# Kernel optimization log

Hardware: AMD Instinct MI355X
Metric: run time of the kernel (lower is better)

The kernel has to match this reference:

```python
import jax, jax.numpy as jnp
import numpy as np

D = H = W = 64
N = D * H * W
BS = 2
C = 32          # enc_dim
IN_DIM = 4
OUT_DIM = 4
P = 5           # pos_enc_dim
COND = 32
M = 8           # modes per axis
NL = 4          # n_layers
NODE_IN = IN_DIM + 3 + 2 * P * 3   # 37
ENC_T = 1 + 2 * P                  # 11
ENC_C = ENC_T * COND               # 352
DT = 0.05


def fourier_embedding(pos, n_freq):
    # F(x) = [cos(2^i*pi*x_l), sin(2^i*pi*x_l)] per coordinate l, then concat x
    freq = (2.0 ** jnp.arange(n_freq, dtype=jnp.float32)) * jnp.pi  # (P,)
    ang = pos[..., None] * freq                                     # (..., L, P)
    emb = jnp.concatenate([jnp.cos(ang), jnp.sin(ang)], axis=-1)    # (..., L, 2P)
    emb = emb.reshape(*pos.shape[:-1], -1)                          # (..., L*2P)
    return jnp.concatenate([emb, pos], axis=-1)


def setup_inputs() -> dict:
    key = jax.random.key(0)
    ks = jax.random.split(key, 24)
    scale = 1.0 / C ** 2
    inp = {
        "state_in": jax.random.normal(ks[0], (BS, N, IN_DIM), jnp.float32),
        "node_pos": jax.random.uniform(ks[1], (BS, N, 3), jnp.float32),
        "edges": jax.random.randint(ks[2], (BS, 16, 2), 0, N),
        "time_i": jax.random.uniform(ks[3], (BS, 1), jnp.float32),
        "conditions": jax.random.uniform(ks[4], (BS, COND), jnp.float32),
        "t_embed_w": jax.random.normal(ks[5], (C, ENC_T), jnp.float32) * 0.05,
        "t_embed_b": jax.random.normal(ks[6], (C,), jnp.float32) * 0.05,
        "c_embed_w": jax.random.normal(ks[7], (C, ENC_C), jnp.float32) * 0.05,
        "c_embed_b": jax.random.normal(ks[8], (C,), jnp.float32) * 0.05,
        "lift_w": jax.random.normal(ks[9], (C, NODE_IN), jnp.float32) * 0.05,
        "lift_b": jax.random.normal(ks[10], (C,), jnp.float32) * 0.05,
        "spec_wr": jax.random.uniform(ks[11], (NL, C, C, M, M, M), jnp.float32) * scale,
        "spec_wi": jax.random.uniform(ks[12], (NL, C, C, M, M, M), jnp.float32) * scale,
        "byp_w": jax.random.normal(ks[13], (NL, C, C), jnp.float32) * 0.05,
        "byp_b": jax.random.normal(ks[14], (NL, C), jnp.float32) * 0.05,
        "proj1_w": jax.random.normal(ks[15], (C, C), jnp.float32) * 0.05,
        "proj1_b": jax.random.normal(ks[16], (C,), jnp.float32) * 0.05,
        "proj2_w": jax.random.normal(ks[17], (OUT_DIM, C), jnp.float32) * 0.05,
        "proj2_b": jax.random.normal(ks[18], (OUT_DIM,), jnp.float32) * 0.05,
    }
    return inp


def _conv1x1(x, w, b):
    # x: (b, c, d, h, w), w: (o, c), b: (o,)
    return jnp.einsum('bcdhw,oc->bodhw', x, w) + b[None, :, None, None, None]


def _fno_forward(state_in, node_pos, time_i, conditions,
                 t_embed_w, t_embed_b, c_embed_w, c_embed_b, lift_w, lift_b,
                 spec_wr, spec_wi, byp_w, byp_b, proj1_w, proj1_b, proj2_w, proj2_b):
    pos_enc = fourier_embedding(node_pos, P)      # (bs, N, 33)
    c_enc = fourier_embedding(conditions, P)      # (bs, 352)
    t_enc = fourier_embedding(time_i, P)          # (bs, 11)

    node_feat = jnp.concatenate([state_in, pos_enc], axis=-1)  # (bs, N, 37)
    t_emb = (t_enc @ t_embed_w.T + t_embed_b)[:, :, None, None, None]
    c_emb = (c_enc @ c_embed_w.T + c_embed_b)[:, :, None, None, None]

    # (bs, N, 37) -> (bs, 37, D, H, W)
    x = node_feat.transpose(0, 2, 1).reshape(BS, NODE_IN, D, H, W)
    x = _conv1x1(x, lift_w, lift_b)
    x = x + t_emb + c_emb

    for l in range(NL):
        w = jax.lax.complex(spec_wr[l], spec_wi[l])              # (C, C, M, M, M)
        x_ft = jnp.fft.rfftn(x, axes=(-3, -2, -1))               # (bs, C, D, H, W//2+1)
        blk = jnp.einsum('bixyz,ioxyz->boxyz', x_ft[..., :M, :M, :M], w)
        out_ft = jnp.zeros_like(x_ft).at[..., :M, :M, :M].set(blk)
        sp = jnp.fft.irfftn(out_ft, s=(D, H, W), axes=(-3, -2, -1))
        bp = _conv1x1(x, byp_w[l], byp_b[l])
        x = jax.nn.gelu(sp + bp, approximate=False)

    x = jax.nn.gelu(_conv1x1(x, proj1_w, proj1_b), approximate=False)
    x = _conv1x1(x, proj2_w, proj2_b)                            # (bs, 4, D, H, W)
    v_pred = x.reshape(BS, OUT_DIM, N).transpose(0, 2, 1)        # (bs, N, 4)
    return state_in + DT * v_pred


def reference(state_in, node_pos, edges, time_i, conditions,
              t_embed_w, t_embed_b, c_embed_w, c_embed_b, lift_w, lift_b,
              spec_wr, spec_wi, byp_w, byp_b, proj1_w, proj1_b, proj2_w, proj2_b):
    # edges are unused in the FNO forward (kept for API compatibility)
    return _fno_forward(state_in, node_pos, time_i, conditions,
                        t_embed_w, t_embed_b, c_embed_w, c_embed_b, lift_w, lift_b,
                        spec_wr, spec_wi, byp_w, byp_b, proj1_w, proj1_b, proj2_w, proj2_b)
```

## Files before the change

### kernel.cpp

```cpp
#include <hip/hip_runtime.h>
#include <math.h>

#define PI_F 3.14159265358979323846f

typedef __bf16 bf16x8 __attribute__((ext_vector_type(8)));
typedef float floatx4 __attribute__((ext_vector_type(4)));
union U8 { unsigned short u[8]; uint4 q; bf16x8 v; };

__device__ __forceinline__ float gelu_sig(float v) {
    float e = __builtin_amdgcn_exp2f(-2.4554670f * v);
    return v * __builtin_amdgcn_rcpf(1.0f + e);
}
__device__ __forceinline__ int rfl(int x) { return __builtin_amdgcn_readfirstlane(x); }

__device__ __forceinline__ unsigned short f2bf(float f) {
    unsigned int u = __float_as_uint(f);
    u += 0x7fffu + ((u >> 16) & 1u);
    return (unsigned short)(u >> 16);
}
__device__ __forceinline__ float bf2f(unsigned short h) {
    return __uint_as_float(((unsigned int)h) << 16);
}
__device__ __forceinline__ unsigned int pack2(float a, float b) {
    return (unsigned int)f2bf(a) | ((unsigned int)f2bf(b) << 16);
}

__global__ void k_wt(const float* __restrict__ time_i, const float* __restrict__ conditions,
                     const float* __restrict__ t_embed_w, const float* __restrict__ t_embed_b,
                     const float* __restrict__ c_embed_w, const float* __restrict__ c_embed_b,
                     const float* __restrict__ lift_b, float* __restrict__ embk,
                     const float* __restrict__ byp_w, const float* __restrict__ lift_w,
                     unsigned short* __restrict__ wbh, unsigned short* __restrict__ wlbf,
                     unsigned short* __restrict__ Tinv, unsigned short* __restrict__ TfT,
                     float* __restrict__ Tp1g, const float* __restrict__ spec_wr,
                     const float* __restrict__ spec_wi, float2* __restrict__ wT) {
    const float th = PI_F / 32.0f;
    __shared__ float red[8][32];
    __shared__ __align__(16) float2 TT[4160];
    int t = threadIdx.x;
    if (blockIdx.x < 2) {
        int b = blockIdx.x;
        int c = t & 31, lg = t >> 5;
        float acc = 0.0f;
        if (lg == 0) {
            acc = t_embed_b[c] + c_embed_b[c] + lift_b[c];
            float tv = time_i[b];
            float ang = PI_F * tv;
            const float* tw = t_embed_w + c * 11;
            for (int i = 0; i < 5; i++) {
                float s, co; sincosf(ang, &s, &co);
                acc += co * tw[i] + s * tw[5 + i];
                ang *= 2.0f;
            }
            acc += tv * tw[10];
        }
        const float* cw = c_embed_w + c * 352;
        for (int j = 0; j < 4; j++) {
            int l = lg * 4 + j;
            float v = conditions[b * 32 + l];
            float ang = PI_F * v;
            for (int i = 0; i < 5; i++) {
                float s, co; sincosf(ang, &s, &co);
                acc += co * cw[l * 10 + i] + s * cw[l * 10 + 5 + i];
                ang *= 2.0f;
            }
            acc += v * cw[320 + l];
        }
        red[lg][c] = acc;
        __syncthreads();
        if (t < 32) {
            float s = 0.0f;
            for (int g = 0; g < 8; g++) s += red[g][t];
            embk[b * 32 + t] = s;
        }
        return;
    }
    if (blockIdx.x >= 40) {
        int n = blockIdx.x - 40;
        int l = n >> 7, i = (n & 127) >> 2, og = n & 3;
        size_t srcb = ((size_t)(l * 1024 + i * 32 + og * 8)) * 512;
        for (int k = 0; k < 16; k++) {
            int e = k * 256 + t;
            TT[(e >> 9) * 520 + (e & 511)] =
                make_float2(spec_wr[srcb + e], spec_wi[srcb + e]);
        }
        __syncthreads();
        for (int k = 0; k < 16; k++) {
            int e = k * 256 + t;
            int o = e & 7, mo = e >> 3;
            int sm = ((mo & 7) << 6) | (mo & 56) | (mo >> 6);
            wT[(size_t)l * 524288 + (size_t)mo * 1024 + i * 32 + og * 8 + o]
                = TT[o * 520 + sm];
        }
        return;
    }
    int idx = (blockIdx.x - 2) * 256 + t;
    if (idx < 4096) {
        wbh[idx] = f2bf(byp_w[idx]);
    } else if (idx < 6144) {
        int j = idx - 4096;
        int o = j >> 6, q = j & 63;
        wlbf[j] = (q < 37) ? f2bf(lift_w[o * 37 + q]) : 0;
    } else if (idx < 8192) {
        int j = idx - 6144;
        int nz = j >> 5, k = j & 31;
        int kz = k >> 1;
        float val = 0.0f;
        if (kz < 8) {
            float a = (float)((kz * nz) & 63) * th;
            val = (k & 1) ? sinf(a) : cosf(a);
            val *= (kz == 0) ? (1.0f / 262144.0f) : (2.0f / 262144.0f);
        }
        Tinv[j] = f2bf(val);
    } else if (idx < 9216) {
        int j = idx - 8192;
        int kcol = j >> 6, nz = j & 63;
        int kz = kcol >> 1;
        float a = (float)((kz * nz) & 63) * th;
        float val = (kcol & 1) ? -sinf(a) : cosf(a);
        TfT[j] = f2bf(val);
    } else if (idx < 9728) {
        int j = idx - 9216;
        int ny = j >> 3, ky = j & 7;
        float a = (float)((ky * ny) & 63) * th;
        Tp1g[j * 2] = cosf(a);
        Tp1g[j * 2 + 1] = sinf(a);
    }
}

__device__ __forceinline__ void swz8k(int blk, int& b, int& nx, int& ny) {
    int x = blk & 7;
    int j = blk >> 3;
    int pair = x * 16 + (j >> 6);
    ny = j & 63;
    b = pair >> 6;
    nx = pair & 63;
}


__global__ __launch_bounds__(256) void k_lift(const float* __restrict__ state_in,
        const float* __restrict__ node_pos, const unsigned short* __restrict__ wlbf,
        const float* __restrict__ embk, const unsigned short* __restrict__ TfT,
        unsigned short* __restrict__ x0, unsigned int* __restrict__ a1) {
    __shared__ __align__(16) float SL[3488];
    unsigned short* fsT  = (unsigned short*)SL;
    unsigned short* ysbf = (unsigned short*)(SL + 2304);
    float* bias = SL + 3456;
    int t = threadIdx.x;
    int b, nx, ny; swz8k(blockIdx.x, b, nx, ny);
    int nxy = nx * 64 + ny;

    if (t < 32) bias[t] = embk[b * 32 + t];
    {
        for (int u = t; u < 2048; u += 256) {
            int row = u >> 5, col = 37 + (u & 31);
            fsT[row * 72 + col] = 0;
        }
    }
    if (t < 192) {
        int nzf = t / 3;
        int l = t - nzf * 3;
        float p = node_pos[((size_t)b * 262144 + (nxy << 6)) * 3 + t];
        float s, c; sincosf(PI_F * p, &s, &c);
        unsigned short* row = fsT + nzf * 72;
        #pragma unroll
        for (int i = 0; i < 5; i++) {
            row[4 + l * 10 + i] = f2bf(c);
            row[4 + l * 10 + 5 + i] = f2bf(s);
            float nc = 2.0f * c * c - 1.0f;
            s = 2.0f * s * c;
            c = nc;
        }
        row[34 + l] = f2bf(p);
    } else {
        int nzf = t - 192;
        const float4 s4 = *(const float4*)(state_in + ((size_t)b * 262144 + (nxy << 6) + nzf) * 4);
        unsigned short* row = fsT + nzf * 72;
        row[0] = f2bf(s4.x); row[1] = f2bf(s4.y);
        row[2] = f2bf(s4.z); row[3] = f2bf(s4.w);
    }
    __syncthreads();

    int lane = t & 63;
    int w = rfl(t >> 6);
    int l15 = lane & 15;
    int quad = lane >> 4;
    int nz = w * 16 + l15;
    size_t xbase = ((size_t)(b * 4096 + nxy)) * 2048;

    U8 b0, b1_;
    b0.q  = *(const uint4*)(fsT + nz * 72 + (quad << 3));
    b1_.q = *(const uint4*)(fsT + nz * 72 + 32 + (quad << 3));
    unsigned short hh[2][4];
    #pragma unroll
    for (int ot = 0; ot < 2; ot++) {
        U8 aA, aB;
        aA.q = *(const uint4*)(wlbf + ((ot * 16 + l15) << 6) + (quad << 3));
        aB.q = *(const uint4*)(wlbf + ((ot * 16 + l15) << 6) + 32 + (quad << 3));
        floatx4 cb;
        #pragma unroll
        for (int r = 0; r < 4; r++) cb[r] = bias[ot * 16 + quad * 4 + r];
        floatx4 d = __builtin_amdgcn_mfma_f32_16x16x32_bf16(aA.v, b0.v, cb, 0, 0, 0);
        d = __builtin_amdgcn_mfma_f32_16x16x32_bf16(aB.v, b1_.v, d, 0, 0, 0);
        #pragma unroll
        for (int r = 0; r < 4; r++) {
            hh[ot][r] = f2bf(d[r]);
            ysbf[(ot * 16 + quad * 4 + r) * 72 + nz] = hh[ot][r];
        }
    }
    *(uint4*)(x0 + xbase + nz * 32 + (quad << 3)) = make_uint4(
        (unsigned)hh[0][0] | ((unsigned)hh[0][1] << 16),
        (unsigned)hh[0][2] | ((unsigned)hh[0][3] << 16),
        (unsigned)hh[1][0] | ((unsigned)hh[1][1] << 16),
        (unsigned)hh[1][2] | ((unsigned)hh[1][3] << 16));
    __syncthreads();

    if (w < 2) {
        int o = w * 16 + l15;
        U8 ay0, ay1, bt0, bt1;
        ay0.q = *(const uint4*)(ysbf + o * 72 + (quad << 3));
        ay1.q = *(const uint4*)(ysbf + o * 72 + 32 + (quad << 3));
        bt0.q = *(const uint4*)(TfT + (l15 << 6) + (quad << 3));
        bt1.q = *(const uint4*)(TfT + (l15 << 6) + 32 + (quad << 3));
        floatx4 z = {0.0f, 0.0f, 0.0f, 0.0f};
        z = __builtin_amdgcn_mfma_f32_16x16x32_bf16(ay0.v, bt0.v, z, 0, 0, 0);
        z = __builtin_amdgcn_mfma_f32_16x16x32_bf16(ay1.v, bt1.v, z, 0, 0, 0);
        float p0 = __shfl_xor(z[0], 1), p1 = __shfl_xor(z[1], 1);
        float p2 = __shfl_xor(z[2], 1), p3 = __shfl_xor(z[3], 1);
        if (!(lane & 1)) {
            unsigned int* a1p = a1 + ((size_t)(b * 4096 + nxy)) * 256;
            int kz = l15 >> 1;
            a1p[(w * 16 + quad * 4 + 0) * 8 + kz] = pack2(z[0], p0);
            a1p[(w * 16 + quad * 4 + 1) * 8 + kz] = pack2(z[1], p1);
            a1p[(w * 16 + quad * 4 + 2) * 8 + kz] = pack2(z[2], p2);
            a1p[(w * 16 + quad * 4 + 3) * 8 + kz] = pack2(z[3], p3);
        }
    }
}


__global__ __launch_bounds__(256) void k_ps1(const unsigned int* __restrict__ a1,
        const float2* __restrict__ Tp1g, float2* __restrict__ a2p) {
    int blk = blockIdx.x, t = threadIdx.x;
    int x = blk & 7, r = blk >> 3;
    int pair = x * 16 + (r & 15);
    int qtr = r >> 4;
    const unsigned int* src = a1 + ((size_t)(pair * 64 + qtr * 16)) * 256 + t;
    float accr[8], acci[8];
    #pragma unroll
    for (int k = 0; k < 8; k++) { accr[k] = 0.0f; acci[k] = 0.0f; }
    #pragma unroll 4
    for (int j = 0; j < 16; j++) {
        int ny = qtr * 16 + j;
        unsigned int pv = src[(size_t)j * 256];
        float vx = bf2f((unsigned short)(pv & 0xffffu));
        float vy = bf2f((unsigned short)(pv >> 16));
        const float2* tw = Tp1g + ny * 8;
        #pragma unroll
        for (int ky = 0; ky < 8; ky++) {
            float2 w2 = tw[ky];
            accr[ky] += vx * w2.x + vy * w2.y;
            acci[ky] += vy * w2.x - vx * w2.y;
        }
    }
    int b = pair >> 6, nx = pair & 63;
    int c = t >> 3, kz = t & 7;
    float2* dst = a2p + ((size_t)((qtr * 2 + b) * 8 + kz)) * 16384 + nx * 32 + c;
    #pragma unroll
    for (int ky = 0; ky < 8; ky++)
        dst[(size_t)ky * 2048] = make_float2(accr[ky], acci[ky]);
}

__global__ __launch_bounds__(256) void k_ps2(const float2* __restrict__ a2p,
        const float2* __restrict__ wTl, const float2* __restrict__ Tp1g,
        float2* __restrict__ b1) {
    __shared__ __align__(16) float2 MS[2048];
    __shared__ __align__(16) float2 XS[256];
    __shared__ __align__(16) float2 YS[288];
    int t = threadIdx.x, blk = blockIdx.x;
    int b = blk >> 6, kz = (blk >> 3) & 7, ky = blk & 7;
    size_t sb = (size_t)b * 131072 + kz * 16384 + ky * 2048;
    for (int k = 0; k < 8; k++) {
        int e = k * 256 + t;
        float2 v0 = a2p[sb + e];
        float2 v1 = a2p[sb + 262144 + e];
        float2 v2 = a2p[sb + 524288 + e];
        float2 v3 = a2p[sb + 786432 + e];
        MS[e] = make_float2(v0.x + v1.x + v2.x + v3.x,
                            v0.y + v1.y + v2.y + v3.y);
    }
    __syncthreads();
    {
        int c = t >> 3, kx = t & 7;
        float sn, cc; sincosf((float)kx * (PI_F / 32.0f), &sn, &cc);
        float bsn = -sn;
        float tc = 1.0f, ts = 0.0f, xr = 0.0f, xi = 0.0f;
        for (int nx = 0; nx < 64; nx++) {
            float2 v = MS[nx * 32 + c];
            xr += v.x * tc - v.y * ts;
            xi += v.x * ts + v.y * tc;
            float nt = tc * cc - ts * bsn; ts = ts * cc + tc * bsn; tc = nt;
        }
        XS[c * 8 + kx] = make_float2(xr, xi);
    }
    __syncthreads();
    {
        int kx = t >> 5, o = t & 31;
        const float2* wp = wTl + ((size_t)(kz * 64 + ky * 8 + kx)) * 1024 + o;
        float yr = 0.0f, yi = 0.0f;
        #pragma unroll 8
        for (int i = 0; i < 32; i++) {
            float2 xv = XS[i * 8 + kx];
            float2 wv = wp[i * 32];
            yr += xv.x * wv.x - xv.y * wv.y;
            yi += xv.x * wv.y + xv.y * wv.x;
        }
        YS[o * 9 + kx] = make_float2(yr, yi);
    }
    __syncthreads();
    {
        int nx8 = t >> 5, o = t & 31;
        for (int j = 0; j < 8; j++) {
            int nx = nx8 * 8 + j;
            const float2* tw = Tp1g + nx * 8;
            float rr = 0.0f, ri = 0.0f;
            #pragma unroll
            for (int kx = 0; kx < 8; kx++) {
                float2 y = YS[o * 9 + kx];
                float2 w2 = tw[kx];
                rr += y.x * w2.x - y.y * w2.y;
                ri += y.x * w2.y + y.y * w2.x;
            }
            b1[((size_t)(b * 64 + nx)) * 2048 + (kz * 8 + ky) * 32 + o]
                = make_float2(rr, ri);
        }
    }
}

__global__ __launch_bounds__(256) void k_fin(
        const unsigned short* __restrict__ xin, const float2* __restrict__ b1,
        const unsigned short* __restrict__ wbh, const float* __restrict__ bb,
        const unsigned short* __restrict__ Tinv, const unsigned short* __restrict__ TfT,
        const float2* __restrict__ Tp1g, unsigned short* __restrict__ xout,
        unsigned int* __restrict__ a1, int do_z, int do_proj,
        const float* __restrict__ state_in, const float* __restrict__ p1w,
        const float* __restrict__ p1b, const float* __restrict__ p2w,
        const float* __restrict__ p2b, float* __restrict__ outp) {
    __shared__ __align__(16) float S[6048];
    float* bstage = S;
    float* pr = S;
    unsigned short* msbf = (unsigned short*)(S + 4224);
    unsigned short* ysbf = (unsigned short*)(S + 4864);
    float* bias = S + 6016;
    int t = threadIdx.x;
    int b, nx, ny; swz8k(blockIdx.x, b, nx, ny);
    int nxy = nx * 64 + ny;
    int lane = t & 63;
    int w = rfl(t >> 6);
    int l15 = lane & 15;
    int quad = lane >> 4;
    int nz = w * 16 + l15;
    size_t xbase = ((size_t)(b * 4096 + nxy)) * 2048;

    int posA = ((quad & 1) << 4) | ((quad >> 1) << 2);
    uint2 xlo = *(const uint2*)(xin + xbase + nz * 32 + posA);
    uint2 xhi = *(const uint2*)(xin + xbase + nz * 32 + posA + 8);
    U8 bx, btv, aw0, aw1;
    ((uint2*)&bx)[0] = xlo; ((uint2*)&bx)[1] = xhi;
    btv.q = *(const uint4*)(Tinv + (nz << 5) + (quad << 3));
    aw0.q = *(const uint4*)(wbh + (l15 << 5) + (quad << 3));
    aw1.q = *(const uint4*)(wbh + ((16 + l15) << 5) + (quad << 3));

    if (t >= 96 && t < 128) bias[t - 96] = bb[t - 96];
    ((unsigned int*)msbf)[(t >> 3) * 20 + 8 + (t & 7)] = 0;

    {
        const float4* b1g = (const float4*)(b1 + ((size_t)(b * 64 + nx)) * 2048);
        #pragma unroll
        for (int j = 0; j < 4; j++) {
            int p = j * 256 + t;
            float4 v = b1g[p];
            int s = p * 2;
            *(float4*)((char*)bstage + s * 8 + ((s >> 6) << 4)) = v;
        }
    }
    __syncthreads();

    {
        int o_ = t >> 3, kz_ = t & 7;
        const float2* tw = Tp1g + ny * 8;
        float mr = 0.0f, mi = 0.0f;
        #pragma unroll
        for (int ky = 0; ky < 8; ky++) {
            int g = kz_ * 256 + ky * 32 + o_;
            float2 v = *(const float2*)((char*)bstage + g * 8 + ((g >> 6) << 4));
            float2 w2 = tw[ky];
            mr += v.x * w2.x - v.y * w2.y;
            mi += v.x * w2.y + v.y * w2.x;
        }
        ((unsigned int*)msbf)[o_ * 20 + kz_] = pack2(mr, -mi);
    }
    __syncthreads();

    U8 am0, am1;
    am0.q = *(const uint4*)(msbf + l15 * 40 + (quad << 3));
    am1.q = *(const uint4*)(msbf + (16 + l15) * 40 + (quad << 3));
    floatx4 cb0, cb1;
    #pragma unroll
    for (int r = 0; r < 4; r++) {
        cb0[r] = bias[quad * 4 + r];
        cb1[r] = bias[16 + quad * 4 + r];
    }
    floatx4 d0 = __builtin_amdgcn_mfma_f32_16x16x32_bf16(aw0.v, bx.v, cb0, 0, 0, 0);
    d0 = __builtin_amdgcn_mfma_f32_16x16x32_bf16(am0.v, btv.v, d0, 0, 0, 0);
    floatx4 d1 = __builtin_amdgcn_mfma_f32_16x16x32_bf16(aw1.v, bx.v, cb1, 0, 0, 0);
    d1 = __builtin_amdgcn_mfma_f32_16x16x32_bf16(am1.v, btv.v, d1, 0, 0, 0);

    unsigned short h0[4], h1[4];
    #pragma unroll
    for (int r = 0; r < 4; r++) {
        h0[r] = f2bf(gelu_sig(d0[r]));
        ysbf[(quad * 4 + r) * 72 + nz] = h0[r];
        h1[r] = f2bf(gelu_sig(d1[r]));
        ysbf[(16 + quad * 4 + r) * 72 + nz] = h1[r];
    }
    if (!do_proj) {
        *(uint4*)(xout + xbase + nz * 32 + (quad << 3)) = make_uint4(
            (unsigned)h0[0] | ((unsigned)h0[1] << 16),
            (unsigned)h0[2] | ((unsigned)h0[3] << 16),
            (unsigned)h1[0] | ((unsigned)h1[1] << 16),
            (unsigned)h1[2] | ((unsigned)h1[3] << 16));
    }
    __syncthreads();

    if (do_z && w < 2) {
        int o = w * 16 + l15;
        U8 ay0, ay1, bt0, bt1;
        ay0.q = *(const uint4*)(ysbf + o * 72 + (quad << 3));
        ay1.q = *(const uint4*)(ysbf + o * 72 + 32 + (quad << 3));
        bt0.q = *(const uint4*)(TfT + (l15 << 6) + (quad << 3));
        bt1.q = *(const uint4*)(TfT + (l15 << 6) + 32 + (quad << 3));
        floatx4 z = {0.0f, 0.0f, 0.0f, 0.0f};
        z = __builtin_amdgcn_mfma_f32_16x16x32_bf16(ay0.v, bt0.v, z, 0, 0, 0);
        z = __builtin_amdgcn_mfma_f32_16x16x32_bf16(ay1.v, bt1.v, z, 0, 0, 0);
        float p0 = __shfl_xor(z[0], 1), p1 = __shfl_xor(z[1], 1);
        float p2 = __shfl_xor(z[2], 1), p3 = __shfl_xor(z[3], 1);
        if (!(lane & 1)) {
            unsigned int* a1p = a1 + ((size_t)(b * 4096 + nxy)) * 256;
            int kz = l15 >> 1;
            a1p[(w * 16 + quad * 4 + 0) * 8 + kz] = pack2(z[0], p0);
            a1p[(w * 16 + quad * 4 + 1) * 8 + kz] = pack2(z[1], p1);
            a1p[(w * 16 + quad * 4 + 2) * 8 + kz] = pack2(z[2], p2);
            a1p[(w * 16 + quad * 4 + 3) * 8 + kz] = pack2(z[3], p3);
        }
    }

    if (do_proj) {
        int nzp = t & 63;
        float xv[32];
        #pragma unroll
        for (int i = 0; i < 32; i++) xv[i] = bf2f(ysbf[i * 72 + nzp]);
        float r0 = 0.f, r1 = 0.f, r2 = 0.f, r3 = 0.f;
        #pragma unroll
        for (int k = 0; k < 8; k++) {
            int o = w * 8 + k;
            float a = p1b[o];
            const float* wr = p1w + o * 32;
            #pragma unroll
            for (int i = 0; i < 32; i++) a += wr[i] * xv[i];
            float h = gelu_sig(a);
            r0 += p2w[0 * 32 + o] * h;
            r1 += p2w[1 * 32 + o] * h;
            r2 += p2w[2 * 32 + o] * h;
            r3 += p2w[3 * 32 + o] * h;
        }
        *(float4*)(pr + w * 256 + nzp * 4) = make_float4(r0, r1, r2, r3);
        __syncthreads();
        if (t < 64) {
            float4 a0 = *(float4*)(pr + 0 * 256 + t * 4);
            float4 a1_ = *(float4*)(pr + 1 * 256 + t * 4);
            float4 a2 = *(float4*)(pr + 2 * 256 + t * 4);
            float4 a3 = *(float4*)(pr + 3 * 256 + t * 4);
            size_t base = ((size_t)b * 262144 + (nxy << 6) + t) * 4;
            float4 sv = *(const float4*)(state_in + base);
            *(float4*)(outp + base) = make_float4(
                sv.x + 0.05f * (p2b[0] + a0.x + a1_.x + a2.x + a3.x),
                sv.y + 0.05f * (p2b[1] + a0.y + a1_.y + a2.y + a3.y),
                sv.z + 0.05f * (p2b[2] + a0.z + a1_.z + a2.z + a3.z),
                sv.w + 0.05f * (p2b[3] + a0.w + a1_.w + a2.w + a3.w));
        }
    }
}

extern "C" void kernel_launch(void* const* d_in, const int* in_sizes, int n_in,
                              void* d_out, int out_size, void* d_ws, size_t ws_size,
                              hipStream_t stream) {
    const float* state_in   = (const float*)d_in[0];
    const float* node_pos   = (const float*)d_in[1];
    const float* time_i     = (const float*)d_in[3];
    const float* conditions = (const float*)d_in[4];
    const float* t_embed_w  = (const float*)d_in[5];
    const float* t_embed_b  = (const float*)d_in[6];
    const float* c_embed_w  = (const float*)d_in[7];
    const float* c_embed_b  = (const float*)d_in[8];
    const float* lift_w     = (const float*)d_in[9];
    const float* lift_b     = (const float*)d_in[10];
    const float* spec_wr    = (const float*)d_in[11];
    const float* spec_wi    = (const float*)d_in[12];
    const float* byp_w      = (const float*)d_in[13];
    const float* byp_b      = (const float*)d_in[14];
    const float* proj1_w    = (const float*)d_in[15];
    const float* proj1_b    = (const float*)d_in[16];
    const float* proj2_w    = (const float*)d_in[17];
    const float* proj2_b    = (const float*)d_in[18];
    float* out = (float*)d_out;
    float* ws  = (float*)d_ws;

    unsigned short* xA = (unsigned short*)ws;
    unsigned short* xB = (unsigned short*)(ws + 8388608);
    unsigned int* a1 = (unsigned int*)(ws + 16777216);
    float2* a2p  = (float2*)(ws + 20971520);
    float2* b1   = (float2*)(ws + 23396352);
    float*  embk = ws + 23920640;
    unsigned short* wbh  = (unsigned short*)(ws + 23920704);
    unsigned short* wlbf = (unsigned short*)(ws + 23922752);
    unsigned short* Tinv = (unsigned short*)(ws + 23923776);
    unsigned short* TfT  = (unsigned short*)(ws + 23924800);
    float* Tp1gf = ws + 23925312;
    float2* Tp1g = (float2*)Tp1gf;
    float2* wT   = (float2*)(ws + 23926336);

    k_wt<<<552, 256, 0, stream>>>(time_i, conditions, t_embed_w, t_embed_b,
                                  c_embed_w, c_embed_b, lift_b, embk,
                                  byp_w, lift_w, wbh, wlbf, Tinv, TfT, Tp1gf,
                                  spec_wr, spec_wi, wT);
    k_lift<<<8192, 256, 0, stream>>>(state_in, node_pos, wlbf, embk, TfT, xA, a1);

    for (int l = 0; l < 4; l++) {
        unsigned short* xin  = (l & 1) ? xB : xA;
        unsigned short* xout = (l & 1) ? xA : xB;
        k_ps1<<<512, 256, 0, stream>>>(a1, Tp1g, a2p);
        k_ps2<<<128, 256, 0, stream>>>(a2p, wT + (size_t)l * 524288, Tp1g, b1);
        k_fin<<<8192, 256, 0, stream>>>(xin, b1, wbh + l * 1024, byp_b + l * 32,
                                        Tinv, TfT, Tp1g, xout, a1, (l < 3) ? 1 : 0,
                                        (l == 3) ? 1 : 0, state_in,
                                        proj1_w, proj1_b, proj2_w, proj2_b, out);
    }
}
```

Baseline: 317.5 us.

## Process four ny rows per k_fin block to reuse staged spectral data

```diff
diff --git a/kernel.cpp b/kernel.cpp
--- a/kernel.cpp
+++ b/kernel.cpp
@@ -346,33 +346,40 @@
         const float* __restrict__ state_in, const float* __restrict__ p1w,
         const float* __restrict__ p1b, const float* __restrict__ p2w,
         const float* __restrict__ p2b, float* __restrict__ outp) {
-    __shared__ __align__(16) float S[6048];
+    __shared__ __align__(16) float S[5248];
     float* bstage = S;
-    float* pr = S;
-    unsigned short* msbf = (unsigned short*)(S + 4224);
-    unsigned short* ysbf = (unsigned short*)(S + 4864);
-    float* bias = S + 6016;
+    unsigned int* msbf = (unsigned int*)(S + 4224);
+    unsigned short* ysbf0 = (unsigned short*)S;
+    unsigned short* ysbf1 = (unsigned short*)(S + 1152);
+    float* pr = S + 2304;
     int t = threadIdx.x;
-    int b, nx, ny; swz8k(blockIdx.x, b, nx, ny);
-    int nxy = nx * 64 + ny;
+    int id = (blockIdx.x & 7) * 256 + (blockIdx.x >> 3);
+    int b = id >> 10, nx = (id >> 4) & 63, nyg = id & 15;
+    int nxy0 = nx * 64 + nyg * 4;
     int lane = t & 63;
     int w = rfl(t >> 6);
     int l15 = lane & 15;
     int quad = lane >> 4;
     int nz = w * 16 + l15;
-    size_t xbase = ((size_t)(b * 4096 + nxy)) * 2048;
+    size_t xbase0 = ((size_t)(b * 4096 + nxy0)) * 2048;
 
     int posA = ((quad & 1) << 4) | ((quad >> 1) << 2);
-    uint2 xlo = *(const uint2*)(xin + xbase + nz * 32 + posA);
-    uint2 xhi = *(const uint2*)(xin + xbase + nz * 32 + posA + 8);
-    U8 bx, btv, aw0, aw1;
-    ((uint2*)&bx)[0] = xlo; ((uint2*)&bx)[1] = xhi;
+    U8 bx[4];
+    #pragma unroll
+    for (int j = 0; j < 4; j++) {
+        ((uint2*)&bx[j])[0] = *(const uint2*)(xin + xbase0 + (size_t)j * 2048 + nz * 32 + posA);
+        ((uint2*)&bx[j])[1] = *(const uint2*)(xin + xbase0 + (size_t)j * 2048 + nz * 32 + posA + 8);
+    }
+    U8 btv, aw0, aw1, bt0, bt1;
     btv.q = *(const uint4*)(Tinv + (nz << 5) + (quad << 3));
     aw0.q = *(const uint4*)(wbh + (l15 << 5) + (quad << 3));
     aw1.q = *(const uint4*)(wbh + ((16 + l15) << 5) + (quad << 3));
-
-    if (t >= 96 && t < 128) bias[t - 96] = bb[t - 96];
-    ((unsigned int*)msbf)[(t >> 3) * 20 + 8 + (t & 7)] = 0;
+    bt0.q = *(const uint4*)(TfT + (l15 << 6) + (quad << 3));
+    bt1.q = *(const uint4*)(TfT + (l15 << 6) + 32 + (quad << 3));
+    float4 c0 = *(const float4*)(bb + quad * 4);
+    float4 c1 = *(const float4*)(bb + 16 + quad * 4);
+    floatx4 cb0 = {c0.x, c0.y, c0.z, c0.w};
+    floatx4 cb1 = {c1.x, c1.y, c1.z, c1.w};
 
     {
         const float4* b1g = (const float4*)(b1 + ((size_t)(b * 64 + nx)) * 2048);
@@ -388,106 +395,117 @@
 
     {
         int o_ = t >> 3, kz_ = t & 7;
-        const float2* tw = Tp1g + ny * 8;
-        float mr = 0.0f, mi = 0.0f;
+        float vr[8], vi[8];
         #pragma unroll
         for (int ky = 0; ky < 8; ky++) {
             int g = kz_ * 256 + ky * 32 + o_;
             float2 v = *(const float2*)((char*)bstage + g * 8 + ((g >> 6) << 4));
-            float2 w2 = tw[ky];
-            mr += v.x * w2.x - v.y * w2.y;
-            mi += v.x * w2.y + v.y * w2.x;
-        }
-        ((unsigned int*)msbf)[o_ * 20 + kz_] = pack2(mr, -mi);
-    }
-    __syncthreads();
-
-    U8 am0, am1;
-    am0.q = *(const uint4*)(msbf + l15 * 40 + (quad << 3));
-    am1.q = *(const uint4*)(msbf + (16 + l15) * 40 + (quad << 3));
-    floatx4 cb0, cb1;
+            vr[ky] = v.x; vi[ky] = v.y;
+        }
+        #pragma unroll
+        for (int j = 0; j < 4; j++) {
+            const float2* tw = Tp1g + (nyg * 4 + j) * 8;
+            float mr = 0.0f, mi = 0.0f;
+            #pragma unroll
+            for (int ky = 0; ky < 8; ky++) {
+                float2 w2 = tw[ky];
+                mr += vr[ky] * w2.x - vi[ky] * w2.y;
+                mi += vr[ky] * w2.y + vi[ky] * w2.x;
+            }
+            msbf[j * 256 + o_ * 8 + kz_] = pack2(mr, -mi);
+        }
+    }
+    __syncthreads();
+
     #pragma unroll
-    for (int r = 0; r < 4; r++) {
-        cb0[r] = bias[quad * 4 + r];
-        cb1[r] = bias[16 + quad * 4 + r];
-    }
-    floatx4 d0 = __builtin_amdgcn_mfma_f32_16x16x32_bf16(aw0.v, bx.v, cb0, 0, 0, 0);
-    d0 = __builtin_amdgcn_mfma_f32_16x16x32_bf16(am0.v, btv.v, d0, 0, 0, 0);
-    floatx4 d1 = __builtin_amdgcn_mfma_f32_16x16x32_bf16(aw1.v, bx.v, cb1, 0, 0, 0);
-    d1 = __builtin_amdgcn_mfma_f32_16x16x32_bf16(am1.v, btv.v, d1, 0, 0, 0);
-
-    unsigned short h0[4], h1[4];
-    #pragma unroll
-    for (int r = 0; r < 4; r++) {
-        h0[r] = f2bf(gelu_sig(d0[r]));
-        ysbf[(quad * 4 + r) * 72 + nz] = h0[r];
-        h1[r] = f2bf(gelu_sig(d1[r]));
-        ysbf[(16 + quad * 4 + r) * 72 + nz] = h1[r];
-    }
-    if (!do_proj) {
-        *(uint4*)(xout + xbase + nz * 32 + (quad << 3)) = make_uint4(
-            (unsigned)h0[0] | ((unsigned)h0[1] << 16),
-            (unsigned)h0[2] | ((unsigned)h0[3] << 16),
-            (unsigned)h1[0] | ((unsigned)h1[1] << 16),
-            (unsigned)h1[2] | ((unsigned)h1[3] << 16));
-    }
-    __syncthreads();
-
-    if (do_z && w < 2) {
-        int o = w * 16 + l15;
-        U8 ay0, ay1, bt0, bt1;
-        ay0.q = *(const uint4*)(ysbf + o * 72 + (quad << 3));
-        ay1.q = *(const uint4*)(ysbf + o * 72 + 32 + (quad << 3));
-        bt0.q = *(const uint4*)(TfT + (l15 << 6) + (quad << 3));
-        bt1.q = *(const uint4*)(TfT + (l15 << 6) + 32 + (quad << 3));
-        floatx4 z = {0.0f, 0.0f, 0.0f, 0.0f};
-        z = __builtin_amdgcn_mfma_f32_16x16x32_bf16(ay0.v, bt0.v, z, 0, 0, 0);
-        z = __builtin_amdgcn_mfma_f32_16x16x32_bf16(ay1.v, bt1.v, z, 0, 0, 0);
-        float p0 = __shfl_xor(z[0], 1), p1 = __shfl_xor(z[1], 1);
-        float p2 = __shfl_xor(z[2], 1), p3 = __shfl_xor(z[3], 1);
-        if (!(lane & 1)) {
-            unsigned int* a1p = a1 + ((size_t)(b * 4096 + nxy)) * 256;
-            int kz = l15 >> 1;
-            a1p[(w * 16 + quad * 4 + 0) * 8 + kz] = pack2(z[0], p0);
-            a1p[(w * 16 + quad * 4 + 1) * 8 + kz] = pack2(z[1], p1);
-            a1p[(w * 16 + quad * 4 + 2) * 8 + kz] = pack2(z[2], p2);
-            a1p[(w * 16 + quad * 4 + 3) * 8 + kz] = pack2(z[3], p3);
-        }
-    }
-
-    if (do_proj) {
-        int nzp = t & 63;
-        float xv[32];
-        #pragma unroll
-        for (int i = 0; i < 32; i++) xv[i] = bf2f(ysbf[i * 72 + nzp]);
-        float r0 = 0.f, r1 = 0.f, r2 = 0.f, r3 = 0.f;
-        #pragma unroll
-        for (int k = 0; k < 8; k++) {
-            int o = w * 8 + k;
-            float a = p1b[o];
-            const float* wr = p1w + o * 32;
+    for (int j = 0; j < 4; j++) {
+        unsigned short* ys = (j & 1) ? ysbf1 : ysbf0;
+        int nxy = nxy0 + j;
+        size_t xbase = xbase0 + (size_t)j * 2048;
+        U8 am0, am1;
+        if (quad < 2) {
+            am0.q = *(const uint4*)(msbf + j * 256 + l15 * 8 + quad * 4);
+            am1.q = *(const uint4*)(msbf + j * 256 + (16 + l15) * 8 + quad * 4);
+        } else {
+            am0.q = make_uint4(0, 0, 0, 0);
+            am1.q = make_uint4(0, 0, 0, 0);
+        }
+        floatx4 d0 = __builtin_amdgcn_mfma_f32_16x16x32_bf16(aw0.v, bx[j].v, cb0, 0, 0, 0);
+        d0 = __builtin_amdgcn_mfma_f32_16x16x32_bf16(am0.v, btv.v, d0, 0, 0, 0);
+        floatx4 d1 = __builtin_amdgcn_mfma_f32_16x16x32_bf16(aw1.v, bx[j].v, cb1, 0, 0, 0);
+        d1 = __builtin_amdgcn_mfma_f32_16x16x32_bf16(am1.v, btv.v, d1, 0, 0, 0);
+
+        unsigned short h0[4], h1[4];
+        #pragma unroll
+        for (int r = 0; r < 4; r++) {
+            h0[r] = f2bf(gelu_sig(d0[r]));
+            ys[(quad * 4 + r) * 72 + nz] = h0[r];
+            h1[r] = f2bf(gelu_sig(d1[r]));
+            ys[(16 + quad * 4 + r) * 72 + nz] = h1[r];
+        }
+        if (!do_proj) {
+            *(uint4*)(xout + xbase + nz * 32 + (quad << 3)) = make_uint4(
+                (unsigned)h0[0] | ((unsigned)h0[1] << 16),
+                (unsigned)h0[2] | ((unsigned)h0[3] << 16),
+                (unsigned)h1[0] | ((unsigned)h1[1] << 16),
+                (unsigned)h1[2] | ((unsigned)h1[3] << 16));
+        }
+        __syncthreads();
+
+        if (do_z) {
+            if (w < 2) {
+                int o = w * 16 + l15;
+                U8 ay0, ay1;
+                ay0.q = *(const uint4*)(ys + o * 72 + (quad << 3));
+                ay1.q = *(const uint4*)(ys + o * 72 + 32 + (quad << 3));
+                floatx4 z = {0.0f, 0.0f, 0.0f, 0.0f};
+                z = __builtin_amdgcn_mfma_f32_16x16x32_bf16(ay0.v, bt0.v, z, 0, 0, 0);
+                z = __builtin_amdgcn_mfma_f32_16x16x32_bf16(ay1.v, bt1.v, z, 0, 0, 0);
+                float p0 = __shfl_xor(z[0], 1), p1 = __shfl_xor(z[1], 1);
+                float p2 = __shfl_xor(z[2], 1), p3 = __shfl_xor(z[3], 1);
+                if (!(lane & 1)) {
+                    unsigned int* a1p = a1 + ((size_t)(b * 4096 + nxy)) * 256;
+                    int kz = l15 >> 1;
+                    a1p[(w * 16 + quad * 4 + 0) * 8 + kz] = pack2(z[0], p0);
+                    a1p[(w * 16 + quad * 4 + 1) * 8 + kz] = pack2(z[1], p1);
+                    a1p[(w * 16 + quad * 4 + 2) * 8 + kz] = pack2(z[2], p2);
+                    a1p[(w * 16 + quad * 4 + 3) * 8 + kz] = pack2(z[3], p3);
+                }
+            }
+        } else if (do_proj) {
+            int nzp = t & 63;
+            float xv[32];
             #pragma unroll
-            for (int i = 0; i < 32; i++) a += wr[i] * xv[i];
-            float h = gelu_sig(a);
-            r0 += p2w[0 * 32 + o] * h;
-            r1 += p2w[1 * 32 + o] * h;
-            r2 += p2w[2 * 32 + o] * h;
-            r3 += p2w[3 * 32 + o] * h;
-        }
-        *(float4*)(pr + w * 256 + nzp * 4) = make_float4(r0, r1, r2, r3);
-        __syncthreads();
-        if (t < 64) {
-            float4 a0 = *(float4*)(pr + 0 * 256 + t * 4);
-            float4 a1_ = *(float4*)(pr + 1 * 256 + t * 4);
-            float4 a2 = *(float4*)(pr + 2 * 256 + t * 4);
-            float4 a3 = *(float4*)(pr + 3 * 256 + t * 4);
-            size_t base = ((size_t)b * 262144 + (nxy << 6) + t) * 4;
-            float4 sv = *(const float4*)(state_in + base);
-            *(float4*)(outp + base) = make_float4(
-                sv.x + 0.05f * (p2b[0] + a0.x + a1_.x + a2.x + a3.x),
-                sv.y + 0.05f * (p2b[1] + a0.y + a1_.y + a2.y + a3.y),
-                sv.z + 0.05f * (p2b[2] + a0.z + a1_.z + a2.z + a3.z),
-                sv.w + 0.05f * (p2b[3] + a0.w + a1_.w + a2.w + a3.w));
+            for (int i = 0; i < 32; i++) xv[i] = bf2f(ys[i * 72 + nzp]);
+            float r0 = 0.f, r1 = 0.f, r2 = 0.f, r3 = 0.f;
+            #pragma unroll
+            for (int k = 0; k < 8; k++) {
+                int o = w * 8 + k;
+                float a = p1b[o];
+                const float* wr = p1w + o * 32;
+                #pragma unroll
+                for (int i = 0; i < 32; i++) a += wr[i] * xv[i];
+                float h = gelu_sig(a);
+                r0 += p2w[0 * 32 + o] * h;
+                r1 += p2w[1 * 32 + o] * h;
+                r2 += p2w[2 * 32 + o] * h;
+                r3 += p2w[3 * 32 + o] * h;
+            }
+            *(float4*)(pr + w * 256 + nzp * 4) = make_float4(r0, r1, r2, r3);
+            __syncthreads();
+            if (t < 64) {
+                float4 a0 = *(float4*)(pr + 0 * 256 + t * 4);
+                float4 a1_ = *(float4*)(pr + 1 * 256 + t * 4);
+                float4 a2 = *(float4*)(pr + 2 * 256 + t * 4);
+                float4 a3 = *(float4*)(pr + 3 * 256 + t * 4);
+                size_t base = ((size_t)b * 262144 + (nxy << 6) + t) * 4;
+                float4 sv = *(const float4*)(state_in + base);
+                *(float4*)(outp + base) = make_float4(
+                    sv.x + 0.05f * (p2b[0] + a0.x + a1_.x + a2.x + a3.x),
+                    sv.y + 0.05f * (p2b[1] + a0.y + a1_.y + a2.y + a3.y),
+                    sv.z + 0.05f * (p2b[2] + a0.z + a1_.z + a2.z + a3.z),
+                    sv.w + 0.05f * (p2b[3] + a0.w + a1_.w + a2.w + a3.w));
+            }
         }
     }
 }
@@ -541,7 +559,7 @@
         unsigned short* xout = (l & 1) ? xA : xB;
         k_ps1<<<512, 256, 0, stream>>>(a1, Tp1g, a2p);
         k_ps2<<<128, 256, 0, stream>>>(a2p, wT + (size_t)l * 524288, Tp1g, b1);
-        k_fin<<<8192, 256, 0, stream>>>(xin, b1, wbh + l * 1024, byp_b + l * 32,
+        k_fin<<<2048, 256, 0, stream>>>(xin, b1, wbh + l * 1024, byp_b + l * 32,
                                         Tinv, TfT, Tp1g, xout, a1, (l < 3) ? 1 : 0,
                                         (l == 3) ? 1 : 0, state_in,
                                         proj1_w, proj1_b, proj2_w, proj2_b, out);
```

After: 318.1 us. Within noise of the previous version (+0.2%).
